# Kernel tuning notes

Hardware: AMD Instinct MI355X
Metric: run time of the kernel (lower is better)

Reference implementation:

```python
import jax, jax.numpy as jnp
import numpy as np
import math

N_LAYERS = 8
D = 1024
H = 16
DK = D // H
T = 1024
V = 32000
B = 2
DFF = 4 * D
EPS = 1e-5


def layernorm(x, scale, bias):
    mu = jnp.mean(x, axis=-1, keepdims=True)
    var = jnp.mean(jnp.square(x - mu), axis=-1, keepdims=True)
    return (x - mu) * jax.lax.rsqrt(var + EPS) * scale + bias


def setup_inputs() -> dict:
    key = jax.random.key(0)
    ks = jax.random.split(key, 32)
    s = 0.02
    rn = lambda k, shape: jax.random.normal(k, shape, dtype=jnp.float32) * s
    x = jax.random.randint(ks[0], (B, T), 0, V)
    return {
        "x": x,
        "inp_emb": rn(ks[1], (V, D)),
        "pos_emb": rn(ks[2], (T, D)),
        # per-layer weights stacked on leading layer axis; per-head wq/wk/wv are
        # concatenated along the output dim (mathematically identical to the
        # per-head nn.Linear list in the torch code)
        "wq": rn(ks[3], (N_LAYERS, D, D)), "bq": jnp.zeros((N_LAYERS, D), jnp.float32),
        "wk": rn(ks[4], (N_LAYERS, D, D)), "bk": jnp.zeros((N_LAYERS, D), jnp.float32),
        "wv": rn(ks[5], (N_LAYERS, D, D)), "bv": jnp.zeros((N_LAYERS, D), jnp.float32),
        "wo": rn(ks[6], (N_LAYERS, D, D)), "bo": jnp.zeros((N_LAYERS, D), jnp.float32),
        "w1": rn(ks[7], (N_LAYERS, D, DFF)), "b1": jnp.zeros((N_LAYERS, DFF), jnp.float32),
        "w2": rn(ks[8], (N_LAYERS, DFF, D)), "b2": jnp.zeros((N_LAYERS, D), jnp.float32),
        "ln1_s": jnp.ones((N_LAYERS, D), jnp.float32), "ln1_b": jnp.zeros((N_LAYERS, D), jnp.float32),
        "ln2_s": jnp.ones((N_LAYERS, D), jnp.float32), "ln2_b": jnp.zeros((N_LAYERS, D), jnp.float32),
        "lno_s": jnp.ones((D,), jnp.float32), "lno_b": jnp.zeros((D,), jnp.float32),
        "w_out": rn(ks[9], (D, V)),
    }


def reference(x, inp_emb, pos_emb, wq, bq, wk, bk, wv, bv, wo, bo,
              w1, b1, w2, b2, ln1_s, ln1_b, ln2_s, ln2_b, lno_s, lno_b, w_out):
    h = inp_emb[x] + pos_emb[jnp.arange(T)]            # [B,T,D]
    causal = jnp.tril(jnp.ones((T, T), dtype=bool))    # [T,T]
    scale = 1.0 / math.sqrt(DK)
    for i in range(N_LAYERS):
        # --- multi-head causal attention ---
        xn = layernorm(h, ln1_s[i], ln1_b[i])
        q = (xn @ wq[i] + bq[i]).reshape(B, T, H, DK)
        k = (xn @ wk[i] + bk[i]).reshape(B, T, H, DK)
        v = (xn @ wv[i] + bv[i]).reshape(B, T, H, DK)
        scores = jnp.einsum('bqhd,bkhd->bhqk', q, k) * scale
        scores = jnp.where(causal, scores, -jnp.inf)
        att = jax.nn.softmax(scores, axis=-1)           # [B,H,T,T]
        y = jnp.einsum('bhqk,bkhd->bqhd', att, v).reshape(B, T, D)
        h = h + y @ wo[i] + bo[i]
        # --- feed-forward ---
        xn = layernorm(h, ln2_s[i], ln2_b[i])
        h = h + jax.nn.gelu(xn @ w1[i] + b1[i], approximate=False) @ w2[i] + b2[i]
    h = layernorm(h, lno_s, lno_b)
    return h @ w_out                                    # logits [B,T,V]
```

## Files before the change

kernel.cpp:

```cpp
#include <hip/hip_runtime.h>
#include <cmath>

#define D_MODEL 1024
#define N_HEADS 16
#define DKH     64
#define SEQ_T   1024
#define BATCH   2
#define VOCAB   32000
#define DFF_    4096
#define NLAYERS 8

typedef __bf16 bf16x8 __attribute__((ext_vector_type(8)));
typedef __bf16 bf16x4v __attribute__((ext_vector_type(4)));
typedef float  f32x4  __attribute__((ext_vector_type(4)));

__device__ __forceinline__ float gelu_f(float x) {
    return 0.5f * x * (1.0f + erff(x * 0.70710678118654752f));
}

__device__ __forceinline__ void gload_lds16(const void* g, void* l) {
    __builtin_amdgcn_global_load_lds(
        (const __attribute__((address_space(1))) void*)g,
        (__attribute__((address_space(3))) void*)l, 16, 0, 0);
}

__global__ __launch_bounds__(256) void embed_kernel(
    const int* __restrict__ x, const float* __restrict__ inp_emb,
    const float* __restrict__ pos_emb, float* __restrict__ h)
{
    const int idx = blockIdx.x * 256 + threadIdx.x;
    const int bt  = idx >> 10;
    const int d   = idx & 1023;
    const int t   = bt & (SEQ_T - 1);
    const int tok = x[bt];
    h[idx] = inp_emb[(size_t)tok * D_MODEL + d] + pos_emb[(size_t)t * D_MODEL + d];
}

__global__ __launch_bounds__(256) void layernorm_kernel(
    const float* __restrict__ x, const float* __restrict__ sc,
    const float* __restrict__ bi, __bf16* __restrict__ o)
{
    const int row = blockIdx.x;
    const int tid = threadIdx.x;
    const int c   = tid * 4;
    const float4 v = *(const float4*)(x + (size_t)row * D_MODEL + c);
    float sum = v.x + v.y + v.z + v.w;
    float sq  = v.x * v.x + v.y * v.y + v.z * v.z + v.w * v.w;
    #pragma unroll
    for (int off = 32; off > 0; off >>= 1) {
        sum += __shfl_xor(sum, off);
        sq  += __shfl_xor(sq, off);
    }
    __shared__ float ssum[4], ssq[4];
    const int wave = tid >> 6, lane = tid & 63;
    if (lane == 0) { ssum[wave] = sum; ssq[wave] = sq; }
    __syncthreads();
    sum = ssum[0] + ssum[1] + ssum[2] + ssum[3];
    sq  = ssq[0]  + ssq[1]  + ssq[2]  + ssq[3];
    const float mu  = sum * (1.0f / D_MODEL);
    const float var = sq * (1.0f / D_MODEL) - mu * mu;
    const float rs  = rsqrtf(var + 1e-5f);
    const float4 s4 = *(const float4*)(sc + c);
    const float4 b4 = *(const float4*)(bi + c);
    bf16x4v ov;
    ov[0] = (__bf16)((v.x - mu) * rs * s4.x + b4.x);
    ov[1] = (__bf16)((v.y - mu) * rs * s4.y + b4.y);
    ov[2] = (__bf16)((v.z - mu) * rs * s4.z + b4.z);
    ov[3] = (__bf16)((v.w - mu) * rs * s4.w + b4.w);
    *(bf16x4v*)(o + (size_t)row * D_MODEL + c) = ov;
}

__global__ __launch_bounds__(256) void prep_layer_kernel(
    const float* __restrict__ wq, const float* __restrict__ wk,
    const float* __restrict__ wv, const float* __restrict__ wo,
    const float* __restrict__ w1, const float* __restrict__ w2,
    const float* __restrict__ bq, const float* __restrict__ bk,
    const float* __restrict__ bv,
    __bf16* __restrict__ wqkvT, __bf16* __restrict__ woT,
    __bf16* __restrict__ w1T, __bf16* __restrict__ w2T,
    float* __restrict__ bqkv)
{
    __shared__ __bf16 tile[32][36];
    const int b   = blockIdx.x;
    const int tid = threadIdx.x;

    if (b >= 12288) {
        const int j = (b - 12288) * 256 + tid;
        bqkv[j] = (j < 1024) ? bq[j] : (j < 2048 ? bk[j - 1024] : bv[j - 2048]);
        return;
    }

    const float* in;
    __bf16* out;
    int K, N, kb0, nb0;
    if (b < 4096) {
        const int w = b >> 10, t = b & 1023;
        K = 1024; N = 1024; kb0 = (t >> 5) * 32; nb0 = (t & 31) * 32;
        in  = (w == 0) ? wq : (w == 1) ? wk : (w == 2) ? wv : wo;
        out = (w == 3) ? woT : wqkvT + (size_t)w * 1024 * 1024;
    } else if (b < 8192) {
        const int t = b - 4096;
        K = 1024; N = 4096; kb0 = (t >> 7) * 32; nb0 = (t & 127) * 32;
        in = w1; out = w1T;
    } else {
        const int t = b - 8192;
        K = 4096; N = 1024; kb0 = (t >> 5) * 32; nb0 = (t & 31) * 32;
        in = w2; out = w2T;
    }

    {
        const int rr = tid >> 3, c4 = (tid & 7) * 4;
        const float4 v = *(const float4*)(in + (size_t)(kb0 + rr) * N + nb0 + c4);
        tile[rr][c4 + 0] = (__bf16)v.x;
        tile[rr][c4 + 1] = (__bf16)v.y;
        tile[rr][c4 + 2] = (__bf16)v.z;
        tile[rr][c4 + 3] = (__bf16)v.w;
    }
    __syncthreads();
    {
        const int cc = tid >> 3, r4 = (tid & 7) * 4;
        bf16x4v ov;
        ov[0] = tile[r4 + 0][cc];
        ov[1] = tile[r4 + 1][cc];
        ov[2] = tile[r4 + 2][cc];
        ov[3] = tile[r4 + 3][cc];
        *(bf16x4v*)(out + (size_t)(nb0 + cc) * K + kb0 + r4) = ov;
    }
}

__global__ __launch_bounds__(256) void wout_tr_kernel(
    const float* __restrict__ in, __bf16* __restrict__ out)
{
    __shared__ __bf16 tile[32][36];
    const int tid = threadIdx.x;
    const int nb0 = (blockIdx.x >> 5) * 32;
    const int kb0 = (blockIdx.x & 31) * 32;
    {
        const int rr = tid >> 3, c4 = (tid & 7) * 4;
        const float4 v = *(const float4*)(in + (size_t)(kb0 + rr) * VOCAB + nb0 + c4);
        tile[rr][c4 + 0] = (__bf16)v.x;
        tile[rr][c4 + 1] = (__bf16)v.y;
        tile[rr][c4 + 2] = (__bf16)v.z;
        tile[rr][c4 + 3] = (__bf16)v.w;
    }
    __syncthreads();
    {
        const int cc = tid >> 3, r4 = (tid & 7) * 4;
        bf16x4v ov;
        ov[0] = tile[r4 + 0][cc];
        ov[1] = tile[r4 + 1][cc];
        ov[2] = tile[r4 + 2][cc];
        ov[3] = tile[r4 + 3][cc];
        *(bf16x4v*)(out + (size_t)(nb0 + cc) * D_MODEL + kb0 + r4) = ov;
    }
}

template <int BN_T, int EPI, typename OutT, bool NT = false>
__global__ __launch_bounds__(256) void gemm_bt(
    const __bf16* __restrict__ A, const __bf16* __restrict__ Bt,
    const float* __restrict__ bias, const float* __restrict__ res,
    OutT* __restrict__ C, int M, int N, int K)
{
    constexpr int NF  = BN_T / 32;
    constexpr int NCB = BN_T / 8;
    __shared__ __bf16 As[128 * 64];
    __shared__ __bf16 Bs[BN_T * 64];

    const int tid  = threadIdx.x;
    const int wave = tid >> 6;
    const int lane = tid & 63;
    const int r    = lane & 15;
    const int kb   = lane >> 4;
    const int wm   = wave >> 1;
    const int wn   = wave & 1;

    const int ntm = gridDim.x;
    const int nwg = ntm * gridDim.y;
    int bid = blockIdx.y * ntm + blockIdx.x;
    if ((nwg & 7) == 0) bid = (bid & 7) * (nwg >> 3) + (bid >> 3);
    const int bm = (bid % ntm) * 128;
    const int bn = (bid / ntm) * BN_T;

    const int srow = lane >> 3;
    const int sg   = lane & 7;

    f32x4 acc[4][NF] = {};

    for (int k0 = 0; k0 < K; k0 += 64) {
        #pragma unroll
        for (int i = 0; i < 4; ++i) {
            const int c    = i * 4 + wave;
            const int row  = c * 8 + srow;
            const int scol = (sg ^ (row & 7)) * 8;
            gload_lds16(A + (size_t)(bm + row) * K + k0 + scol, &As[c * 512]);
        }
        #pragma unroll
        for (int i = 0; i < NCB / 4; ++i) {
            const int c    = i * 4 + wave;
            const int row  = c * 8 + srow;
            const int scol = (sg ^ (row & 7)) * 8;
            gload_lds16(Bt + (size_t)(bn + row) * K + k0 + scol, &Bs[c * 512]);
        }
        __syncthreads();

        #pragma unroll
        for (int s = 0; s < 2; ++s) {
            bf16x8 af[4];
            #pragma unroll
            for (int m = 0; m < 4; ++m) {
                const int row = wm * 64 + m * 16 + r;
                const int g   = (s * 4 + kb) ^ (row & 7);
                af[m] = *(const bf16x8*)&As[row * 64 + g * 8];
            }
            #pragma unroll
            for (int n = 0; n < NF; ++n) {
                const int row = wn * (NF * 16) + n * 16 + r;
                const int g   = (s * 4 + kb) ^ (row & 7);
                const bf16x8 bfr = *(const bf16x8*)&Bs[row * 64 + g * 8];
                #pragma unroll
                for (int m = 0; m < 4; ++m)
                    acc[m][n] = __builtin_amdgcn_mfma_f32_16x16x32_bf16(af[m], bfr, acc[m][n], 0, 0, 0);
            }
        }
        __syncthreads();
    }

    #pragma unroll
    for (int m = 0; m < 4; ++m) {
        const int row = bm + wm * 64 + m * 16 + kb * 4;
        #pragma unroll
        for (int n = 0; n < NF; ++n) {
            const int col = bn + wn * (NF * 16) + n * 16 + r;
            const float bv = bias ? bias[col] : 0.0f;
            #pragma unroll
            for (int rg = 0; rg < 4; ++rg) {
                float v = acc[m][n][rg] + bv;
                if constexpr (EPI == 1) v += res[(size_t)(row + rg) * N + col];
                if constexpr (EPI == 2) v = gelu_f(v);
                if constexpr (NT) {
                    __builtin_nontemporal_store((OutT)v, &C[(size_t)(row + rg) * N + col]);
                } else {
                    C[(size_t)(row + rg) * N + col] = (OutT)v;
                }
            }
        }
    }
}

__global__ __launch_bounds__(512) void attn_mfma_kernel(
    const __bf16* __restrict__ qkv, __bf16* __restrict__ y)
{
    constexpr int QS = 3 * D_MODEL;
    __shared__ __align__(16) __bf16 K_lds[64][72];
    __shared__ __align__(16) __bf16 V_lds[64][72];
    __shared__ __align__(16) __bf16 P_lds[8][16][72];

    const int tid  = threadIdx.x;
    const int wave = tid >> 6;
    const int lane = tid & 63;
    const int r    = lane & 15;
    const int kb   = lane >> 4;

    const int q0 = blockIdx.x * 128;
    const int b  = blockIdx.y >> 4;
    const int h  = blockIdx.y & 15;

    const __bf16* qp = qkv + (size_t)b * SEQ_T * QS + h * DKH;
    const __bf16* kp = qp + D_MODEL;
    const __bf16* vp = qp + 2 * D_MODEL;
    __bf16* yp = y + (size_t)b * SEQ_T * D_MODEL + h * DKH;

    bf16x8 qf[2];
    {
        const int qrow = q0 + wave * 16 + r;
        #pragma unroll
        for (int kc = 0; kc < 2; ++kc)
            qf[kc] = *(const bf16x8*)(qp + (size_t)qrow * QS + kc * 32 + kb * 8);
    }

    float m_run[4] = {-INFINITY, -INFINITY, -INFINITY, -INFINITY};
    float l_run[4] = {0.0f, 0.0f, 0.0f, 0.0f};
    f32x4 yacc[4] = {};

    const int skey = tid >> 3;
    const int sg8  = (tid & 7) * 8;

    const int ntiles = (q0 >> 6) + 2;
    for (int kt = 0; kt < ntiles; ++kt) {
        {
            const size_t go = (size_t)(kt * 64 + skey) * QS;
            *(bf16x8*)&K_lds[skey][sg8] = *(const bf16x8*)(kp + go + sg8);
            const bf16x8 vv = *(const bf16x8*)(vp + go + sg8);
            const int swz = (sg8 >> 3) * 8;
            #pragma unroll
            for (int j = 0; j < 8; ++j)
                V_lds[sg8 + j][skey ^ swz] = vv[j];
        }
        __syncthreads();

        f32x4 sacc[4] = {};
        #pragma unroll
        for (int kc = 0; kc < 2; ++kc) {
            #pragma unroll
            for (int g = 0; g < 4; ++g) {
                const bf16x8 kf = *(const bf16x8*)&K_lds[g * 16 + r][kc * 32 + kb * 8];
                sacc[g] = __builtin_amdgcn_mfma_f32_16x16x32_bf16(qf[kc], kf, sacc[g], 0, 0, 0);
            }
        }

        float s[4][4], p[4][4];
        #pragma unroll
        for (int g = 0; g < 4; ++g) {
            const int key = kt * 64 + g * 16 + r;
            #pragma unroll
            for (int rg = 0; rg < 4; ++rg) {
                const int qq = q0 + wave * 16 + kb * 4 + rg;
                s[g][rg] = (key <= qq) ? sacc[g][rg] * 0.125f : -INFINITY;
            }
        }
        float mt[4], mn[4], corr[4], psum[4];
        #pragma unroll
        for (int rg = 0; rg < 4; ++rg)
            mt[rg] = fmaxf(fmaxf(s[0][rg], s[1][rg]), fmaxf(s[2][rg], s[3][rg]));
        #pragma unroll
        for (int off = 1; off < 16; off <<= 1) {
            #pragma unroll
            for (int rg = 0; rg < 4; ++rg) mt[rg] = fmaxf(mt[rg], __shfl_xor(mt[rg], off));
        }
        #pragma unroll
        for (int rg = 0; rg < 4; ++rg) {
            mn[rg]  = fmaxf(m_run[rg], mt[rg]);
            psum[rg] = 0.0f;
            #pragma unroll
            for (int g = 0; g < 4; ++g) {
                p[g][rg] = __expf(s[g][rg] - mn[rg]);
                psum[rg] += p[g][rg];
            }
        }
        #pragma unroll
        for (int off = 1; off < 16; off <<= 1) {
            #pragma unroll
            for (int rg = 0; rg < 4; ++rg) psum[rg] += __shfl_xor(psum[rg], off);
        }
        #pragma unroll
        for (int rg = 0; rg < 4; ++rg) {
            corr[rg] = __expf(m_run[rg] - mn[rg]);
            l_run[rg] = l_run[rg] * corr[rg] + psum[rg];
            m_run[rg] = mn[rg];
        }
        #pragma unroll
        for (int n = 0; n < 4; ++n) {
            #pragma unroll
            for (int rg = 0; rg < 4; ++rg) yacc[n][rg] *= corr[rg];
        }

        #pragma unroll
        for (int g = 0; g < 4; ++g) {
            #pragma unroll
            for (int rg = 0; rg < 4; ++rg)
                P_lds[wave][kb * 4 + rg][g * 16 + r] = (__bf16)p[g][rg];
        }
        const bf16x8 pa0 = *(const bf16x8*)&P_lds[wave][r][kb * 8];
        const bf16x8 pa1 = *(const bf16x8*)&P_lds[wave][r][32 + kb * 8];

        #pragma unroll
        for (int n = 0; n < 4; ++n) {
            const int vrow = n * 16 + r;
            const int swz  = (vrow >> 3) & 7;
            const bf16x8 vf0 = *(const bf16x8*)&V_lds[vrow][(kb ^ swz) * 8];
            yacc[n] = __builtin_amdgcn_mfma_f32_16x16x32_bf16(pa0, vf0, yacc[n], 0, 0, 0);
        }
        #pragma unroll
        for (int n = 0; n < 4; ++n) {
            const int vrow = n * 16 + r;
            const int swz  = (vrow >> 3) & 7;
            const bf16x8 vf1 = *(const bf16x8*)&V_lds[vrow][((kb + 4) ^ swz) * 8];
            yacc[n] = __builtin_amdgcn_mfma_f32_16x16x32_bf16(pa1, vf1, yacc[n], 0, 0, 0);
        }
        __syncthreads();
    }

    float inv[4];
    #pragma unroll
    for (int rg = 0; rg < 4; ++rg) inv[rg] = 1.0f / l_run[rg];
    #pragma unroll
    for (int n = 0; n < 4; ++n) {
        #pragma unroll
        for (int rg = 0; rg < 4; ++rg) {
            const int row = q0 + wave * 16 + kb * 4 + rg;
            yp[(size_t)row * D_MODEL + n * 16 + r] = (__bf16)(yacc[n][rg] * inv[rg]);
        }
    }
}

extern "C" void kernel_launch(void* const* d_in, const int* in_sizes, int n_in,
                              void* d_out, int out_size, void* d_ws, size_t ws_size,
                              hipStream_t stream)
{
    const int*   x       = (const int*)  d_in[0];
    const float* inp_emb = (const float*)d_in[1];
    const float* pos_emb = (const float*)d_in[2];
    const float* wq = (const float*)d_in[3];
    const float* bq = (const float*)d_in[4];
    const float* wk = (const float*)d_in[5];
    const float* bk = (const float*)d_in[6];
    const float* wv = (const float*)d_in[7];
    const float* bv = (const float*)d_in[8];
    const float* wo = (const float*)d_in[9];
    const float* bo = (const float*)d_in[10];
    const float* w1 = (const float*)d_in[11];
    const float* b1 = (const float*)d_in[12];
    const float* w2 = (const float*)d_in[13];
    const float* b2 = (const float*)d_in[14];
    const float* ln1_s = (const float*)d_in[15];
    const float* ln1_b = (const float*)d_in[16];
    const float* ln2_s = (const float*)d_in[17];
    const float* ln2_b = (const float*)d_in[18];
    const float* lno_s = (const float*)d_in[19];
    const float* lno_b = (const float*)d_in[20];
    const float* w_out = (const float*)d_in[21];

    const int M = BATCH * SEQ_T;
    const size_t MB = 1u << 20;

    char* w = (char*)d_ws;
    float*  h     = (float*) (w + 0);
    __bf16* xn    = (__bf16*)(w + 8  * MB);
    __bf16* yb    = (__bf16*)(w + 12 * MB);
    __bf16* sh    = (__bf16*)(w + 16 * MB);
    __bf16* wqkvT = (__bf16*)(w + 32 * MB);
    __bf16* woT   = (__bf16*)(w + 38 * MB);
    __bf16* w1T   = (__bf16*)(w + 40 * MB);
    __bf16* w2T   = (__bf16*)(w + 48 * MB);
    float*  bqkv  = (float*) (w + 56 * MB);
    __bf16* woutT = (__bf16*)(w + 57 * MB);

    embed_kernel<<<dim3(M * D_MODEL / 256), 256, 0, stream>>>(x, inp_emb, pos_emb, h);

    for (int i = 0; i < NLAYERS; ++i) {
        const size_t wOff  = (size_t)i * D_MODEL * D_MODEL;
        const size_t w1Off = (size_t)i * D_MODEL * DFF_;

        prep_layer_kernel<<<dim3(12300), 256, 0, stream>>>(
            wq + wOff, wk + wOff, wv + wOff, wo + wOff, w1 + w1Off, w2 + w1Off,
            bq + i * D_MODEL, bk + i * D_MODEL, bv + i * D_MODEL,
            wqkvT, woT, w1T, w2T, bqkv);

        layernorm_kernel<<<dim3(M), 256, 0, stream>>>(h, ln1_s + i * D_MODEL, ln1_b + i * D_MODEL, xn);
        gemm_bt<128, 0, __bf16><<<dim3(M / 128, 3 * D_MODEL / 128), 256, 0, stream>>>(
            xn, wqkvT, bqkv, nullptr, sh, M, 3 * D_MODEL, D_MODEL);
        attn_mfma_kernel<<<dim3(SEQ_T / 128, BATCH * N_HEADS), 512, 0, stream>>>(sh, yb);
        gemm_bt<64, 1, float><<<dim3(M / 128, D_MODEL / 64), 256, 0, stream>>>(
            yb, woT, bo + i * D_MODEL, h, h, M, D_MODEL, D_MODEL);
        layernorm_kernel<<<dim3(M), 256, 0, stream>>>(h, ln2_s + i * D_MODEL, ln2_b + i * D_MODEL, xn);
        gemm_bt<128, 2, __bf16><<<dim3(M / 128, DFF_ / 128), 256, 0, stream>>>(
            xn, w1T, b1 + i * DFF_, nullptr, sh, M, DFF_, D_MODEL);
        gemm_bt<64, 1, float><<<dim3(M / 128, D_MODEL / 64), 256, 0, stream>>>(
            sh, w2T, b2 + i * D_MODEL, h, h, M, D_MODEL, DFF_);
    }

    wout_tr_kernel<<<dim3((VOCAB / 32) * 32), 256, 0, stream>>>(w_out, woutT);
    layernorm_kernel<<<dim3(M), 256, 0, stream>>>(h, lno_s, lno_b, xn);
    gemm_bt<128, 0, float, true><<<dim3(M / 128, VOCAB / 128), 256, 0, stream>>>(
        xn, woutT, nullptr, nullptr, (float*)d_out, M, VOCAB, D_MODEL);
}
```

Measured before the change: 1.831 ms.

## Balance causal attention work by pairing mirrored query tiles per block

```diff
diff --git a/kernel.cpp b/kernel.cpp
--- a/kernel.cpp
+++ b/kernel.cpp
@@ -247,13 +247,106 @@
     }
 }
 
-__global__ __launch_bounds__(512) void attn_mfma_kernel(
+struct AttnState {
+    float m[4];
+    float l[4];
+    f32x4 yacc[4];
+};
+
+__device__ __forceinline__ void attn_tile_step(
+    AttnState& st, const bf16x8 (&qf)[2], int q0, int kt,
+    int wave, int r, int kb,
+    const __bf16 (*K_lds)[72], const __bf16 (*V_lds)[72],
+    __bf16 (*P_row)[72])
+{
+    f32x4 sacc[4] = {};
+    #pragma unroll
+    for (int kc = 0; kc < 2; ++kc) {
+        #pragma unroll
+        for (int g = 0; g < 4; ++g) {
+            const bf16x8 kf = *(const bf16x8*)&K_lds[g * 16 + r][kc * 32 + kb * 8];
+            sacc[g] = __builtin_amdgcn_mfma_f32_16x16x32_bf16(qf[kc], kf, sacc[g], 0, 0, 0);
+        }
+    }
+
+    float s[4][4], p[4][4];
+    #pragma unroll
+    for (int g = 0; g < 4; ++g) {
+        const int key = kt * 64 + g * 16 + r;
+        #pragma unroll
+        for (int rg = 0; rg < 4; ++rg) {
+            const int qq = q0 + wave * 16 + kb * 4 + rg;
+            s[g][rg] = (key <= qq) ? sacc[g][rg] * 0.125f : -INFINITY;
+        }
+    }
+    float mt[4], mn[4], corr[4], psum[4];
+    #pragma unroll
+    for (int rg = 0; rg < 4; ++rg)
+        mt[rg] = fmaxf(fmaxf(s[0][rg], s[1][rg]), fmaxf(s[2][rg], s[3][rg]));
+    #pragma unroll
+    for (int off = 1; off < 16; off <<= 1) {
+        #pragma unroll
+        for (int rg = 0; rg < 4; ++rg) mt[rg] = fmaxf(mt[rg], __shfl_xor(mt[rg], off));
+    }
+    #pragma unroll
+    for (int rg = 0; rg < 4; ++rg) {
+        mn[rg]  = fmaxf(st.m[rg], mt[rg]);
+        psum[rg] = 0.0f;
+        #pragma unroll
+        for (int g = 0; g < 4; ++g) {
+            p[g][rg] = __expf(s[g][rg] - mn[rg]);
+            psum[rg] += p[g][rg];
+        }
+    }
+    #pragma unroll
+    for (int off = 1; off < 16; off <<= 1) {
+        #pragma unroll
+        for (int rg = 0; rg < 4; ++rg) psum[rg] += __shfl_xor(psum[rg], off);
+    }
+    #pragma unroll
+    for (int rg = 0; rg < 4; ++rg) {
+        corr[rg] = __expf(st.m[rg] - mn[rg]);
+        st.l[rg] = st.l[rg] * corr[rg] + psum[rg];
+        st.m[rg] = mn[rg];
+    }
+    #pragma unroll
+    for (int n = 0; n < 4; ++n) {
+        #pragma unroll
+        for (int rg = 0; rg < 4; ++rg) st.yacc[n][rg] *= corr[rg];
+    }
+
+    #pragma unroll
+    for (int g = 0; g < 4; ++g) {
+        #pragma unroll
+        for (int rg = 0; rg < 4; ++rg)
+            P_row[kb * 4 + rg][g * 16 + r] = (__bf16)p[g][rg];
+    }
+    const bf16x8 pa0 = *(const bf16x8*)&P_row[r][kb * 8];
+    const bf16x8 pa1 = *(const bf16x8*)&P_row[r][32 + kb * 8];
+
+    #pragma unroll
+    for (int n = 0; n < 4; ++n) {
+        const int vrow = n * 16 + r;
+        const int swz  = (vrow >> 3) & 7;
+        const bf16x8 vf0 = *(const bf16x8*)&V_lds[vrow][(kb ^ swz) * 8];
+        st.yacc[n] = __builtin_amdgcn_mfma_f32_16x16x32_bf16(pa0, vf0, st.yacc[n], 0, 0, 0);
+    }
+    #pragma unroll
+    for (int n = 0; n < 4; ++n) {
+        const int vrow = n * 16 + r;
+        const int swz  = (vrow >> 3) & 7;
+        const bf16x8 vf1 = *(const bf16x8*)&V_lds[vrow][((kb + 4) ^ swz) * 8];
+        st.yacc[n] = __builtin_amdgcn_mfma_f32_16x16x32_bf16(pa1, vf1, st.yacc[n], 0, 0, 0);
+    }
+}
+
+__global__ __launch_bounds__(256) void attn_mfma_kernel(
     const __bf16* __restrict__ qkv, __bf16* __restrict__ y)
 {
     constexpr int QS = 3 * D_MODEL;
     __shared__ __align__(16) __bf16 K_lds[64][72];
     __shared__ __align__(16) __bf16 V_lds[64][72];
-    __shared__ __align__(16) __bf16 P_lds[8][16][72];
+    __shared__ __align__(16) __bf16 P_lds[4][16][72];
 
     const int tid  = threadIdx.x;
     const int wave = tid >> 6;
@@ -261,134 +354,79 @@
     const int r    = lane & 15;
     const int kb   = lane >> 4;
 
-    const int q0 = blockIdx.x * 128;
-    const int b  = blockIdx.y >> 4;
-    const int h  = blockIdx.y & 15;
+    const int ip  = blockIdx.x;
+    const int q0A = ip * 64;
+    const int q0B = (15 - ip) * 64;
+    const int b   = blockIdx.y >> 4;
+    const int h   = blockIdx.y & 15;
 
     const __bf16* qp = qkv + (size_t)b * SEQ_T * QS + h * DKH;
     const __bf16* kp = qp + D_MODEL;
     const __bf16* vp = qp + 2 * D_MODEL;
     __bf16* yp = y + (size_t)b * SEQ_T * D_MODEL + h * DKH;
 
-    bf16x8 qf[2];
+    bf16x8 qfA[2], qfB[2];
     {
-        const int qrow = q0 + wave * 16 + r;
-        #pragma unroll
-        for (int kc = 0; kc < 2; ++kc)
-            qf[kc] = *(const bf16x8*)(qp + (size_t)qrow * QS + kc * 32 + kb * 8);
-    }
-
-    float m_run[4] = {-INFINITY, -INFINITY, -INFINITY, -INFINITY};
-    float l_run[4] = {0.0f, 0.0f, 0.0f, 0.0f};
-    f32x4 yacc[4] = {};
-
-    const int skey = tid >> 3;
-    const int sg8  = (tid & 7) * 8;
-
-    const int ntiles = (q0 >> 6) + 2;
+        const int qrA = q0A + wave * 16 + r;
+        const int qrB = q0B + wave * 16 + r;
+        #pragma unroll
+        for (int kc = 0; kc < 2; ++kc) {
+            qfA[kc] = *(const bf16x8*)(qp + (size_t)qrA * QS + kc * 32 + kb * 8);
+            qfB[kc] = *(const bf16x8*)(qp + (size_t)qrB * QS + kc * 32 + kb * 8);
+        }
+    }
+
+    AttnState stA, stB;
+    #pragma unroll
+    for (int rg = 0; rg < 4; ++rg) {
+        stA.m[rg] = -INFINITY; stA.l[rg] = 0.0f;
+        stB.m[rg] = -INFINITY; stB.l[rg] = 0.0f;
+    }
+    #pragma unroll
+    for (int n = 0; n < 4; ++n) { stA.yacc[n] = {}; stB.yacc[n] = {}; }
+
+    const int skey = tid >> 2;
+    const int sg16 = (tid & 3) * 16;
+
+    const int ntiles = 16 - ip;
     for (int kt = 0; kt < ntiles; ++kt) {
         {
             const size_t go = (size_t)(kt * 64 + skey) * QS;
-            *(bf16x8*)&K_lds[skey][sg8] = *(const bf16x8*)(kp + go + sg8);
-            const bf16x8 vv = *(const bf16x8*)(vp + go + sg8);
-            const int swz = (sg8 >> 3) * 8;
+            *(bf16x8*)&K_lds[skey][sg16]     = *(const bf16x8*)(kp + go + sg16);
+            *(bf16x8*)&K_lds[skey][sg16 + 8] = *(const bf16x8*)(kp + go + sg16 + 8);
+            const bf16x8 v0 = *(const bf16x8*)(vp + go + sg16);
+            const bf16x8 v1 = *(const bf16x8*)(vp + go + sg16 + 8);
+            const int swz0 = ((sg16 >> 3) & 7) * 8;
+            const int swz1 = (((sg16 + 8) >> 3) & 7) * 8;
             #pragma unroll
             for (int j = 0; j < 8; ++j)
-                V_lds[sg8 + j][skey ^ swz] = vv[j];
+                V_lds[sg16 + j][skey ^ swz0] = v0[j];
+            #pragma unroll
+            for (int j = 0; j < 8; ++j)
+                V_lds[sg16 + 8 + j][skey ^ swz1] = v1[j];
         }
         __syncthreads();
 
-        f32x4 sacc[4] = {};
-        #pragma unroll
-        for (int kc = 0; kc < 2; ++kc) {
-            #pragma unroll
-            for (int g = 0; g < 4; ++g) {
-                const bf16x8 kf = *(const bf16x8*)&K_lds[g * 16 + r][kc * 32 + kb * 8];
-                sacc[g] = __builtin_amdgcn_mfma_f32_16x16x32_bf16(qf[kc], kf, sacc[g], 0, 0, 0);
-            }
-        }
-
-        float s[4][4], p[4][4];
-        #pragma unroll
-        for (int g = 0; g < 4; ++g) {
-            const int key = kt * 64 + g * 16 + r;
-            #pragma unroll
-            for (int rg = 0; rg < 4; ++rg) {
-                const int qq = q0 + wave * 16 + kb * 4 + rg;
-                s[g][rg] = (key <= qq) ? sacc[g][rg] * 0.125f : -INFINITY;
-            }
-        }
-        float mt[4], mn[4], corr[4], psum[4];
-        #pragma unroll
-        for (int rg = 0; rg < 4; ++rg)
-            mt[rg] = fmaxf(fmaxf(s[0][rg], s[1][rg]), fmaxf(s[2][rg], s[3][rg]));
-        #pragma unroll
-        for (int off = 1; off < 16; off <<= 1) {
-            #pragma unroll
-            for (int rg = 0; rg < 4; ++rg) mt[rg] = fmaxf(mt[rg], __shfl_xor(mt[rg], off));
-        }
+        attn_tile_step(stB, qfB, q0B, kt, wave, r, kb, K_lds, V_lds, P_lds[wave]);
+        if (kt <= ip)
+            attn_tile_step(stA, qfA, q0A, kt, wave, r, kb, K_lds, V_lds, P_lds[wave]);
+        __syncthreads();
+    }
+
+    float invA[4], invB[4];
+    #pragma unroll
+    for (int rg = 0; rg < 4; ++rg) {
+        invA[rg] = 1.0f / stA.l[rg];
+        invB[rg] = 1.0f / stB.l[rg];
+    }
+    #pragma unroll
+    for (int n = 0; n < 4; ++n) {
         #pragma unroll
         for (int rg = 0; rg < 4; ++rg) {
-            mn[rg]  = fmaxf(m_run[rg], mt[rg]);
-            psum[rg] = 0.0f;
-            #pragma unroll
-            for (int g = 0; g < 4; ++g) {
-                p[g][rg] = __expf(s[g][rg] - mn[rg]);
-                psum[rg] += p[g][rg];
-            }
-        }
-        #pragma unroll
-        for (int off = 1; off < 16; off <<= 1) {
-            #pragma unroll
-            for (int rg = 0; rg < 4; ++rg) psum[rg] += __shfl_xor(psum[rg], off);
-        }
-        #pragma unroll
-        for (int rg = 0; rg < 4; ++rg) {
-            corr[rg] = __expf(m_run[rg] - mn[rg]);
-            l_run[rg] = l_run[rg] * corr[rg] + psum[rg];
-            m_run[rg] = mn[rg];
-        }
-        #pragma unroll
-        for (int n = 0; n < 4; ++n) {
-            #pragma unroll
-            for (int rg = 0; rg < 4; ++rg) yacc[n][rg] *= corr[rg];
-        }
-
-        #pragma unroll
-        for (int g = 0; g < 4; ++g) {
-            #pragma unroll
-            for (int rg = 0; rg < 4; ++rg)
-                P_lds[wave][kb * 4 + rg][g * 16 + r] = (__bf16)p[g][rg];
-        }
-        const bf16x8 pa0 = *(const bf16x8*)&P_lds[wave][r][kb * 8];
-        const bf16x8 pa1 = *(const bf16x8*)&P_lds[wave][r][32 + kb * 8];
-
-        #pragma unroll
-        for (int n = 0; n < 4; ++n) {
-            const int vrow = n * 16 + r;
-            const int swz  = (vrow >> 3) & 7;
-            const bf16x8 vf0 = *(const bf16x8*)&V_lds[vrow][(kb ^ swz) * 8];
-            yacc[n] = __builtin_amdgcn_mfma_f32_16x16x32_bf16(pa0, vf0, yacc[n], 0, 0, 0);
-        }
-        #pragma unroll
-        for (int n = 0; n < 4; ++n) {
-            const int vrow = n * 16 + r;
-            const int swz  = (vrow >> 3) & 7;
-            const bf16x8 vf1 = *(const bf16x8*)&V_lds[vrow][((kb + 4) ^ swz) * 8];
-            yacc[n] = __builtin_amdgcn_mfma_f32_16x16x32_bf16(pa1, vf1, yacc[n], 0, 0, 0);
-        }
-        __syncthreads();
-    }
-
-    float inv[4];
-    #pragma unroll
-    for (int rg = 0; rg < 4; ++rg) inv[rg] = 1.0f / l_run[rg];
-    #pragma unroll
-    for (int n = 0; n < 4; ++n) {
-        #pragma unroll
-        for (int rg = 0; rg < 4; ++rg) {
-            const int row = q0 + wave * 16 + kb * 4 + rg;
-            yp[(size_t)row * D_MODEL + n * 16 + r] = (__bf16)(yacc[n][rg] * inv[rg]);
+            const int rowA = q0A + wave * 16 + kb * 4 + rg;
+            const int rowB = q0B + wave * 16 + kb * 4 + rg;
+            yp[(size_t)rowA * D_MODEL + n * 16 + r] = (__bf16)(stA.yacc[n][rg] * invA[rg]);
+            yp[(size_t)rowB * D_MODEL + n * 16 + r] = (__bf16)(stB.yacc[n][rg] * invB[rg]);
         }
     }
 }
@@ -449,7 +487,7 @@
         layernorm_kernel<<<dim3(M), 256, 0, stream>>>(h, ln1_s + i * D_MODEL, ln1_b + i * D_MODEL, xn);
         gemm_bt<128, 0, __bf16><<<dim3(M / 128, 3 * D_MODEL / 128), 256, 0, stream>>>(
             xn, wqkvT, bqkv, nullptr, sh, M, 3 * D_MODEL, D_MODEL);
-        attn_mfma_kernel<<<dim3(SEQ_T / 128, BATCH * N_HEADS), 512, 0, stream>>>(sh, yb);
+        attn_mfma_kernel<<<dim3(8, BATCH * N_HEADS), 256, 0, stream>>>(sh, yb);
         gemm_bt<64, 1, float><<<dim3(M / 128, D_MODEL / 64), 256, 0, stream>>>(
             yb, woT, bo + i * D_MODEL, h, h, M, D_MODEL, D_MODEL);
         layernorm_kernel<<<dim3(M), 256, 0, stream>>>(h, ln2_s + i * D_MODEL, ln2_b + i * D_MODEL, xn);
```

Result: faster. 1.712 ms (-6.5%).
